# Optimization experiments

Hardware: AMD Instinct MI355X
Metric: run time of the kernel (lower is better)

The kernel has to match this reference:

```python
import jax, jax.numpy as jnp
import numpy as np

B, N_OBJ, N_REL = 32, 100, 512
D_OBJ, D_CTX, D_HID = 1024, 1024, 1024


def setup_inputs() -> dict:
    key = jax.random.key(0)
    k1, k2, k3, k4, k5 = jax.random.split(key, 5)
    object_branch_output = jax.random.normal(k1, (B * N_OBJ, D_OBJ), dtype=jnp.float32)
    context_branch_output = jax.random.normal(k2, (B, D_CTX), dtype=jnp.float32)
    num_obj = jnp.full((B,), N_OBJ, dtype=jnp.int32)
    num_rels = jnp.full((B,), N_REL, dtype=jnp.int32)
    obj_pairs = jax.random.randint(k3, (B, N_REL, 2), 0, N_OBJ, dtype=jnp.int32)
    W1 = jax.random.normal(k4, (D_OBJ + D_CTX, D_HID), dtype=jnp.float32) * (1.0 / np.sqrt(D_OBJ + D_CTX))
    b1 = jnp.zeros((D_HID,), dtype=jnp.float32)
    W2 = jax.random.normal(k5, (D_HID, D_HID), dtype=jnp.float32) * (1.0 / np.sqrt(D_HID))
    b2 = jnp.zeros((D_HID,), dtype=jnp.float32)
    return {
        "object_branch_output": object_branch_output,
        "context_branch_output": context_branch_output,
        "num_obj": num_obj,
        "num_rels": num_rels,
        "obj_pairs": obj_pairs,
        "W1": W1, "b1": b1, "W2": W2, "b2": b2,
    }


def reference(object_branch_output, context_branch_output, num_obj, num_rels,
              obj_pairs, W1, b1, W2, b2):
    # --- prepare_f_oo_vis_input, fully vectorized ---
    # per-batch object index offsets: sum(num_obj[:b])  (exclusive cumsum)
    obj_offsets = jnp.cumsum(num_obj) - num_obj                       # [B]
    global_pairs = obj_pairs + obj_offsets[:, None, None]             # [B, R, 2]
    # gather both endpoints of every pair and mean-aggregate
    pair_feats = object_branch_output[global_pairs]                   # [B, R, 2, D_obj]
    obj_vec = pair_feats.mean(axis=2)                                 # [B, R, D_obj]
    # broadcast per-batch context vector to every relation, then concat
    ctx = jnp.broadcast_to(context_branch_output[:, None, :],
                           obj_vec.shape[:2] + (context_branch_output.shape[-1],))
    input_f_oo_vis = jnp.concatenate([obj_vec, ctx], axis=-1)         # [B, R, D_obj+D_ctx]
    x = input_f_oo_vis.reshape(-1, input_f_oo_vis.shape[-1])          # [tot_rels, D_obj+D_ctx]
    # --- f_oo_vis MLP: (Linear -> ReLU) per layer pair ---
    h = jax.nn.relu(x @ W1 + b1)
    f_oo_vis_output = jax.nn.relu(h @ W2 + b2)
    return object_branch_output, f_oo_vis_output
```

## Files before the change

### kernel.cpp

```cpp
#include <hip/hip_runtime.h>
#include <hip/hip_bf16.h>

#define BB   32
#define NREL 512
#define DD   1024
#define MTOT (BB * NREL)
#define OBJ_ROWS (BB * 100)
#define PPLANE ((size_t)OBJ_ROWS * DD)

typedef __attribute__((ext_vector_type(8))) short bf16x8;
typedef __attribute__((ext_vector_type(4))) float f32x4;

__device__ __forceinline__ unsigned short f2bf(float f) {
    union { float f; unsigned u; } v; v.f = f;
    unsigned r = v.u + 0x7fff + ((v.u >> 16) & 1);
    return (unsigned short)(r >> 16);
}

__device__ __forceinline__ float bf2f(unsigned short s) {
    union { unsigned u; float f; } v; v.u = (unsigned)s << 16;
    return v.f;
}

__device__ __forceinline__ void gld16(const void* g, void* l) {
    __builtin_amdgcn_global_load_lds(
        (const __attribute__((address_space(1))) unsigned int*)g,
        (__attribute__((address_space(3))) unsigned int*)l,
        16, 0, 0);
}

__device__ __forceinline__ void barfence() {
    asm volatile("" ::: "memory");
    __builtin_amdgcn_s_barrier();
    asm volatile("" ::: "memory");
}

__global__ void __launch_bounds__(256) prep_kernel(
    const float* __restrict__ obj, const float* __restrict__ ctx,
    const float* __restrict__ W1, const float* __restrict__ W2,
    unsigned short* __restrict__ W1t, unsigned short* __restrict__ W2t,
    float* __restrict__ part, unsigned short* __restrict__ obj_bf,
    float* __restrict__ out_obj) {
    __shared__ float smem[32 * 33];
    int bid = blockIdx.x;
    int tid = threadIdx.x;

    if (bid < 1024) {
        int slice = bid & 3, chunk = (bid >> 2) & 7, b = bid >> 5;
        int nl = tid & 127, kh = tid >> 7;
        int n = chunk * 128 + nl;
        int kbase = slice * 256 + kh * 128;
        const float* c = ctx + (size_t)b * DD + kbase;
        const float* w = W1 + (size_t)(DD + kbase) * DD + n;
        float a0 = 0.f, a1 = 0.f, a2 = 0.f, a3 = 0.f;
#pragma unroll 8
        for (int k = 0; k < 128; k += 4) {
            a0 = fmaf(c[k + 0], w[(size_t)(k + 0) * DD], a0);
            a1 = fmaf(c[k + 1], w[(size_t)(k + 1) * DD], a1);
            a2 = fmaf(c[k + 2], w[(size_t)(k + 2) * DD], a2);
            a3 = fmaf(c[k + 3], w[(size_t)(k + 3) * DD], a3);
        }
        smem[kh * 128 + nl] = (a0 + a1) + (a2 + a3);
        __syncthreads();
        if (kh == 0)
            part[(((size_t)slice * BB + b) << 10) + n] = smem[nl] + smem[128 + nl];
    } else if (bid < 3072) {
        const float* W = (bid < 2048) ? W1 : W2;
        unsigned short* Wt = (bid < 2048) ? W1t : W2t;
        int t = (bid - 1024) & 1023;
        int k0 = (t >> 5) * 32, n0 = (t & 31) * 32;
        int tr = tid >> 5, tc = tid & 31;
#pragma unroll
        for (int i = 0; i < 4; i++)
            smem[(tr + i * 8) * 33 + tc] = W[(size_t)(k0 + tr + i * 8) * DD + n0 + tc];
        __syncthreads();
#pragma unroll
        for (int i = 0; i < 4; i++)
            Wt[(size_t)(n0 + tr + i * 8) * DD + k0 + tc] = f2bf(smem[tc * 33 + tr + i * 8]);
    } else {
        const float4* src = (const float4*)obj;
        float4* dst = (float4*)out_obj;
        ushort4* dbf = (ushort4*)obj_bf;
        for (int i = (bid - 3072) * 256 + tid; i < OBJ_ROWS * DD / 4; i += 2048 * 256) {
            float4 v = src[i];
            dst[i] = v;
            ushort4 o;
            o.x = f2bf(v.x); o.y = f2bf(v.y); o.z = f2bf(v.z); o.w = f2bf(v.w);
            dbf[i] = o;
        }
    }
}

__global__ void __launch_bounds__(256) gemmP_kernel(
    const unsigned short* __restrict__ A,
    const unsigned short* __restrict__ Bt,
    unsigned short* __restrict__ P,
    const float* __restrict__ part,
    const float* __restrict__ b1,
    float* __restrict__ cbias) {
    constexpr int K = 1024;
    __shared__ __attribute__((aligned(16))) unsigned short As[128 * 32];
    __shared__ __attribute__((aligned(16))) unsigned short Bs[128 * 32];
    int bid = blockIdx.x;
    int tid = threadIdx.x;

    if (bid >= 400) {
        int b = bid - 400;
        float4 v = ((const float4*)b1)[tid];
#pragma unroll
        for (int s = 0; s < 4; s++) {
            float4 p = ((const float4*)(part + (((size_t)s * BB + b) << 10)))[tid];
            v.x += p.x; v.y += p.y; v.z += p.z; v.w += p.w;
        }
        ((float4*)(cbias + ((size_t)b << 10)))[tid] = v;
        return;
    }

    int ks = bid / 200;
    int t200 = bid - ks * 200;
    int lane = tid & 63, wave = tid >> 6;
    int wr = wave >> 1, wc = wave & 1;
    int mBase = (t200 >> 3) * 128;
    int nBase = (t200 & 7) * 128;
    int kLo = ks * 512, kHi = kLo + 512;

    f32x4 acc[4][4];
#pragma unroll
    for (int i = 0; i < 4; i++)
#pragma unroll
        for (int j = 0; j < 4; j++) acc[i][j] = (f32x4){0.f, 0.f, 0.f, 0.f};

    const unsigned short* Ab = A + (size_t)mBase * K;
    const unsigned short* Bb = Bt + (size_t)nBase * K;

    for (int k0 = kLo; k0 < kHi; k0 += 32) {
#pragma unroll
        for (int hh = 0; hh < 2; hh++) {
            int c = tid + hh * 256;
            int row = c >> 2, kc = (c & 3) * 8;
            gld16(Ab + (size_t)row * K + k0 + kc, As + c * 8);
            gld16(Bb + (size_t)row * K + k0 + kc, Bs + c * 8);
        }
        __syncthreads();
        int lr = lane & 15, kg = (lane >> 4) * 8;
        bf16x8 af[4], bfr[4];
#pragma unroll
        for (int m = 0; m < 4; m++)
            af[m] = *(const bf16x8*)&As[(wr * 64 + m * 16 + lr) * 32 + kg];
#pragma unroll
        for (int n = 0; n < 4; n++)
            bfr[n] = *(const bf16x8*)&Bs[(wc * 64 + n * 16 + lr) * 32 + kg];
#pragma unroll
        for (int m = 0; m < 4; m++)
#pragma unroll
            for (int n = 0; n < 4; n++)
                acc[m][n] = __builtin_amdgcn_mfma_f32_16x16x32_bf16(af[m], bfr[n], acc[m][n], 0, 0, 0);
        __syncthreads();
    }

    unsigned short* Pk = P + (size_t)ks * PPLANE;
    int lr = lane & 15, rg = (lane >> 4) * 4;
#pragma unroll
    for (int m = 0; m < 4; m++)
#pragma unroll
        for (int n = 0; n < 4; n++) {
            int col = nBase + wc * 64 + n * 16 + lr;
#pragma unroll
            for (int r = 0; r < 4; r++) {
                int row = mBase + wr * 64 + m * 16 + rg + r;
                Pk[(size_t)row * DD + col] = f2bf(acc[m][n][r]);
            }
        }
}

__global__ void __launch_bounds__(256) hgen_kernel(
    const unsigned short* __restrict__ P, const int* __restrict__ pairs,
    const int* __restrict__ num_obj, const float* __restrict__ cbias,
    unsigned short* __restrict__ h) {
    int rbase = blockIdx.x * 4;
    int b = rbase >> 9;
    int off = 0;
    for (int i = 0; i < b; i++) off += num_obj[i];
    int t = threadIdx.x;

    float4 bv = ((const float4*)(cbias + ((size_t)b << 10)))[t];
    const unsigned short* P1 = P + PPLANE;

#pragma unroll
    for (int rr = 0; rr < 4; rr++) {
        int row = rbase + rr;
        int i0 = pairs[2 * row] + off;
        int i1 = pairs[2 * row + 1] + off;
        ushort4 a0 = ((const ushort4*)(P  + (size_t)i0 * DD))[t];
        ushort4 a1 = ((const ushort4*)(P1 + (size_t)i0 * DD))[t];
        ushort4 c0 = ((const ushort4*)(P  + (size_t)i1 * DD))[t];
        ushort4 c1 = ((const ushort4*)(P1 + (size_t)i1 * DD))[t];
        float v0 = 0.5f * ((bf2f(a0.x) + bf2f(a1.x)) + (bf2f(c0.x) + bf2f(c1.x))) + bv.x;
        float v1 = 0.5f * ((bf2f(a0.y) + bf2f(a1.y)) + (bf2f(c0.y) + bf2f(c1.y))) + bv.y;
        float v2 = 0.5f * ((bf2f(a0.z) + bf2f(a1.z)) + (bf2f(c0.z) + bf2f(c1.z))) + bv.z;
        float v3 = 0.5f * ((bf2f(a0.w) + bf2f(a1.w)) + (bf2f(c0.w) + bf2f(c1.w))) + bv.w;
        ushort4 o;
        o.x = f2bf(v0 > 0.f ? v0 : 0.f);
        o.y = f2bf(v1 > 0.f ? v1 : 0.f);
        o.z = f2bf(v2 > 0.f ? v2 : 0.f);
        o.w = f2bf(v3 > 0.f ? v3 : 0.f);
        ((ushort4*)(h + (size_t)row * DD))[t] = o;
    }
}

__global__ void __launch_bounds__(512, 2) gemm2_kernel(
    const unsigned short* __restrict__ A,
    const unsigned short* __restrict__ Bt,
    const float* __restrict__ bias,
    float* __restrict__ Cout) {
    constexpr int K = 1024;
    constexpr int NT = K / 64;
    extern __shared__ unsigned short lds[];
    int tid = threadIdx.x;
    int lane = tid & 63, wave = tid >> 6;
    int wr = wave >> 2, wc = wave & 3;
    int lr = lane & 15, g = lane >> 4;

    int wg = blockIdx.x;
    int swz = (wg & 7) * 32 + (wg >> 3);
    int mBase = (swz >> 2) * 256;
    int nBase = (swz & 3) * 256;

    const unsigned short* Ab = A + (size_t)mBase * K;
    const unsigned short* Bb = Bt + (size_t)nBase * K;

    int srow[4], soff[4], sdst[4];
#pragma unroll
    for (int i = 0; i < 4; i++) {
        int s = i * 512 + tid;
        int row = s >> 3, cperm = s & 7;
        srow[i] = row;
        soff[i] = (cperm ^ (row & 7)) * 8;
        sdst[i] = s * 8;
    }

    f32x4 acc[8][4];
#pragma unroll
    for (int i = 0; i < 8; i++)
#pragma unroll
        for (int j = 0; j < 4; j++) acc[i][j] = (f32x4){0.f, 0.f, 0.f, 0.f};

    auto STAGE = [&](int bi, int kt) {
        unsigned short* Ad = lds + bi * 16384;
        unsigned short* Bd = lds + 32768 + bi * 16384;
        int ko = kt * 64;
#pragma unroll
        for (int i = 0; i < 4; i++) {
            gld16(Ab + (size_t)srow[i] * K + ko + soff[i], Ad + sdst[i]);
            gld16(Bb + (size_t)srow[i] * K + ko + soff[i], Bd + sdst[i]);
        }
    };

    auto COMPUTE = [&](int bi) {
        const unsigned short* As = lds + bi * 16384;
        const unsigned short* Bs = lds + 32768 + bi * 16384;
        bf16x8 bfr[4][2];
#pragma unroll
        for (int n = 0; n < 4; n++)
#pragma unroll
            for (int kk = 0; kk < 2; kk++) {
                int row = wc * 64 + n * 16 + lr;
                int c = kk * 4 + g;
                bfr[n][kk] = *(const bf16x8*)&Bs[row * 64 + ((c ^ (row & 7)) * 8)];
            }
#pragma unroll
        for (int half = 0; half < 2; half++) {
            bf16x8 af[4][2];
#pragma unroll
            for (int m = 0; m < 4; m++)
#pragma unroll
                for (int kk = 0; kk < 2; kk++) {
                    int row = wr * 128 + (half * 4 + m) * 16 + lr;
                    int c = kk * 4 + g;
                    af[m][kk] = *(const bf16x8*)&As[row * 64 + ((c ^ (row & 7)) * 8)];
                }
            __builtin_amdgcn_s_setprio(1);
#pragma unroll
            for (int m = 0; m < 4; m++)
#pragma unroll
                for (int n = 0; n < 4; n++)
#pragma unroll
                    for (int kk = 0; kk < 2; kk++)
                        acc[half * 4 + m][n] = __builtin_amdgcn_mfma_f32_16x16x32_bf16(
                            af[m][kk], bfr[n][kk], acc[half * 4 + m][n], 0, 0, 0);
            __builtin_amdgcn_s_setprio(0);
        }
    };

    STAGE(0, 0);
    int cur = 0;
    for (int kt = 0; kt < NT - 1; ++kt) {
        STAGE(cur ^ 1, kt + 1);
        asm volatile("s_waitcnt vmcnt(8)" ::: "memory");
        barfence();
        COMPUTE(cur);
        barfence();
        cur ^= 1;
    }
    asm volatile("s_waitcnt vmcnt(0)" ::: "memory");
    barfence();
    COMPUTE(cur);

    int rg = g * 4;
#pragma unroll
    for (int m = 0; m < 8; m++) {
#pragma unroll
        for (int n = 0; n < 4; n++) {
            int col = nBase + wc * 64 + n * 16 + lr;
            float bv = bias[col];
#pragma unroll
            for (int r = 0; r < 4; r++) {
                int row = mBase + wr * 128 + m * 16 + rg + r;
                float v = acc[m][n][r] + bv;
                Cout[(size_t)row * 1024 + col] = v > 0.f ? v : 0.f;
            }
        }
    }
}

extern "C" void kernel_launch(void* const* d_in, const int* in_sizes, int n_in,
                              void* d_out, int out_size, void* d_ws, size_t ws_size,
                              hipStream_t stream) {
    (void)in_sizes; (void)n_in; (void)out_size; (void)ws_size;
    const float* obj     = (const float*)d_in[0];
    const float* ctx     = (const float*)d_in[1];
    const int*   num_obj = (const int*)d_in[2];
    const int*   pairs   = (const int*)d_in[4];
    const float* W1      = (const float*)d_in[5];
    const float* b1      = (const float*)d_in[6];
    const float* W2      = (const float*)d_in[7];
    const float* b2      = (const float*)d_in[8];

    char* ws = (char*)d_ws;
    unsigned short* obj_bf = (unsigned short*)(ws);
    unsigned short* P      = (unsigned short*)(ws + 6553600);
    unsigned short* h      = (unsigned short*)(ws + 19660800);
    unsigned short* W1t    = (unsigned short*)(ws + 53215232);
    unsigned short* W2t    = (unsigned short*)(ws + 55312384);
    float*          cbias  = (float*)(ws + 57409536);

    float* out_obj = (float*)d_out;
    float* out_f   = out_obj + (size_t)OBJ_ROWS * DD;
    float* part    = out_f;

    hipFuncSetAttribute(reinterpret_cast<const void*>(gemm2_kernel),
                        hipFuncAttributeMaxDynamicSharedMemorySize, 131072);

    prep_kernel<<<dim3(5120), 256, 0, stream>>>(
        obj, ctx, W1, W2, W1t, W2t, part, obj_bf, out_obj);
    gemmP_kernel<<<dim3(432), 256, 0, stream>>>(obj_bf, W1t, P, part, b1, cbias);
    hgen_kernel<<<dim3(4096), 256, 0, stream>>>(P, pairs, num_obj, cbias, h);
    gemm2_kernel<<<dim3(256), 512, 131072, stream>>>(h, W2t, b2, out_f);
}
```

Measured before the change: 89.86 us.

## Move W2 transpose and object passthrough copy into gemmP launch

Moves the W2 transpose-to-bf16 work and the fp32 object-output copy out of the prep kernel and into extra blocks of the gemmP launch. Those blocks are independent of the first GEMM, so they can fill idle compute units while the 400 GEMM tiles run, and the prep kernel on the critical path gets shorter. The risk is that the extra memory-bound blocks compete with GEMM tiles for bandwidth and scheduling slots, and a larger grid may delay when GEMM blocks get dispatched.

```diff
diff --git a/kernel.cpp b/kernel.cpp
--- a/kernel.cpp
+++ b/kernel.cpp
@@ -37,10 +37,9 @@
 
 __global__ void __launch_bounds__(256) prep_kernel(
     const float* __restrict__ obj, const float* __restrict__ ctx,
-    const float* __restrict__ W1, const float* __restrict__ W2,
-    unsigned short* __restrict__ W1t, unsigned short* __restrict__ W2t,
-    float* __restrict__ part, unsigned short* __restrict__ obj_bf,
-    float* __restrict__ out_obj) {
+    const float* __restrict__ W1,
+    unsigned short* __restrict__ W1t,
+    float* __restrict__ part, unsigned short* __restrict__ obj_bf) {
     __shared__ float smem[32 * 33];
     int bid = blockIdx.x;
     int tid = threadIdx.x;
@@ -64,26 +63,22 @@
         __syncthreads();
         if (kh == 0)
             part[(((size_t)slice * BB + b) << 10) + n] = smem[nl] + smem[128 + nl];
-    } else if (bid < 3072) {
-        const float* W = (bid < 2048) ? W1 : W2;
-        unsigned short* Wt = (bid < 2048) ? W1t : W2t;
-        int t = (bid - 1024) & 1023;
+    } else if (bid < 2048) {
+        int t = bid - 1024;
         int k0 = (t >> 5) * 32, n0 = (t & 31) * 32;
         int tr = tid >> 5, tc = tid & 31;
 #pragma unroll
         for (int i = 0; i < 4; i++)
-            smem[(tr + i * 8) * 33 + tc] = W[(size_t)(k0 + tr + i * 8) * DD + n0 + tc];
+            smem[(tr + i * 8) * 33 + tc] = W1[(size_t)(k0 + tr + i * 8) * DD + n0 + tc];
         __syncthreads();
 #pragma unroll
         for (int i = 0; i < 4; i++)
-            Wt[(size_t)(n0 + tr + i * 8) * DD + k0 + tc] = f2bf(smem[tc * 33 + tr + i * 8]);
+            W1t[(size_t)(n0 + tr + i * 8) * DD + k0 + tc] = f2bf(smem[tc * 33 + tr + i * 8]);
     } else {
         const float4* src = (const float4*)obj;
-        float4* dst = (float4*)out_obj;
         ushort4* dbf = (ushort4*)obj_bf;
-        for (int i = (bid - 3072) * 256 + tid; i < OBJ_ROWS * DD / 4; i += 2048 * 256) {
+        for (int i = (bid - 2048) * 256 + tid; i < OBJ_ROWS * DD / 4; i += 1024 * 256) {
             float4 v = src[i];
-            dst[i] = v;
             ushort4 o;
             o.x = f2bf(v.x); o.y = f2bf(v.y); o.z = f2bf(v.z); o.w = f2bf(v.w);
             dbf[i] = o;
@@ -97,13 +92,38 @@
     unsigned short* __restrict__ P,
     const float* __restrict__ part,
     const float* __restrict__ b1,
-    float* __restrict__ cbias) {
+    float* __restrict__ cbias,
+    const float* __restrict__ obj,
+    const float* __restrict__ W2,
+    unsigned short* __restrict__ W2t,
+    float* __restrict__ out_obj) {
     constexpr int K = 1024;
     __shared__ __attribute__((aligned(16))) unsigned short As[128 * 32];
     __shared__ __attribute__((aligned(16))) unsigned short Bs[128 * 32];
     int bid = blockIdx.x;
     int tid = threadIdx.x;
 
+    if (bid >= 1456) {
+        const float4* src = (const float4*)obj;
+        float4* dst = (float4*)out_obj;
+        for (int i = (bid - 1456) * 256 + tid; i < OBJ_ROWS * DD / 4; i += 2048 * 256)
+            dst[i] = src[i];
+        return;
+    }
+    if (bid >= 432) {
+        float* tile = (float*)As;
+        int t = bid - 432;
+        int k0 = (t >> 5) * 32, n0 = (t & 31) * 32;
+        int tr = tid >> 5, tc = tid & 31;
+#pragma unroll
+        for (int i = 0; i < 4; i++)
+            tile[(tr + i * 8) * 33 + tc] = W2[(size_t)(k0 + tr + i * 8) * DD + n0 + tc];
+        __syncthreads();
+#pragma unroll
+        for (int i = 0; i < 4; i++)
+            W2t[(size_t)(n0 + tr + i * 8) * DD + k0 + tc] = f2bf(tile[tc * 33 + tr + i * 8]);
+        return;
+    }
     if (bid >= 400) {
         int b = bid - 400;
         float4 v = ((const float4*)b1)[tid];
@@ -351,9 +371,10 @@
     hipFuncSetAttribute(reinterpret_cast<const void*>(gemm2_kernel),
                         hipFuncAttributeMaxDynamicSharedMemorySize, 131072);
 
-    prep_kernel<<<dim3(5120), 256, 0, stream>>>(
-        obj, ctx, W1, W2, W1t, W2t, part, obj_bf, out_obj);
-    gemmP_kernel<<<dim3(432), 256, 0, stream>>>(obj_bf, W1t, P, part, b1, cbias);
+    prep_kernel<<<dim3(3072), 256, 0, stream>>>(
+        obj, ctx, W1, W1t, part, obj_bf);
+    gemmP_kernel<<<dim3(3504), 256, 0, stream>>>(
+        obj_bf, W1t, P, part, b1, cbias, obj, W2, W2t, out_obj);
     hgen_kernel<<<dim3(4096), 256, 0, stream>>>(P, pairs, num_obj, cbias, h);
     gemm2_kernel<<<dim3(256), 512, 131072, stream>>>(h, W2t, b2, out_f);
 }
```

After: 90.06 us. Within noise of the previous version (+0.2%).
